# Kernel tuning notes

Measured on AMD Instinct MI355X. Metric: run time of the kernel, lower is better.

Reference implementation:

```python
import jax, jax.numpy as jnp
import numpy as np
from math import sqrt

N_PATCHES = 128
ATTENTION_WINDOW = 10
NEG_FILL = -10000.0


def _mask(L):
    # pid[i] = patch index of position i; channels = L // n_patches
    channels = L // N_PATCHES
    pid = jnp.repeat(jnp.arange(N_PATCHES), channels)
    diff = pid[None, :] - pid[:, None]  # diff[i, j] = pid[j] - pid[i]
    return (diff <= 0) | (diff >= ATTENTION_WINDOW)  # True = masked


def setup_inputs() -> dict:
    key = jax.random.key(0)
    k1, k2, k3 = jax.random.split(key, 3)
    B, H, L, D = 4, 8, 2048, 64
    return {
        "queries": jax.random.normal(k1, (B, H, L, D), dtype=jnp.float32),
        "keys": jax.random.normal(k2, (B, H, L, D), dtype=jnp.float32),
        "values": jax.random.normal(k3, (B, H, L, D), dtype=jnp.float32),
        "log_scale": jnp.asarray(np.log(2.0), dtype=jnp.float32),
    }


def reference(queries, keys, values, log_scale):
    B, H, L, D = queries.shape
    scores = jnp.einsum("bhqd,bhkd->bhqk", queries, keys)
    scale = jnp.clip(jnp.exp(log_scale), 1.0, 30.0) / sqrt(D)
    cmask = _mask(L)[None, None]  # [1,1,L,L]
    pos = jnp.where(cmask, NEG_FILL, scores)
    neg = jnp.where(cmask, NEG_FILL, -scores)
    A = jax.nn.softmax(scale * pos, axis=-1) - jax.nn.softmax(scale * neg, axis=-1)
    return jnp.einsum("bhqk,bhkd->bhqd", A, values)
```

## Files before the change

kernel.cpp:

```cpp
#include <hip/hip_runtime.h>
#include <hip/hip_bf16.h>


#define LSEQ   2048
#define DIM    64
#define CH     16
#define WIN    9
#define GRP    8
#define VCOLS  272

#define SK 72
#define SV 280
#define SA 168
#define UNELEMS 21504

typedef __attribute__((ext_vector_type(8))) short bf16x8;
typedef __attribute__((ext_vector_type(4))) float f32x4;

__device__ __forceinline__ unsigned short f2bf1(float a) {
  unsigned int u = __float_as_uint(a);
  u = (u + 0x7fffu + ((u >> 16) & 1u)) >> 16;
  return (unsigned short)u;
}

__device__ __forceinline__ unsigned int pack2bf(float a, float b) {
  unsigned int ua = __float_as_uint(a);
  unsigned int ub = __float_as_uint(b);
  ua = (ua + 0x7fffu + ((ua >> 16) & 1u)) >> 16;
  ub = (ub + 0x7fffu + ((ub >> 16) & 1u)) & 0xffff0000u;
  return ua | ub;
}

__device__ __forceinline__ bf16x8 pack8(float4 a, float4 b) {
  bf16x8 r;
  r[0] = (short)f2bf1(a.x); r[1] = (short)f2bf1(a.y);
  r[2] = (short)f2bf1(a.z); r[3] = (short)f2bf1(a.w);
  r[4] = (short)f2bf1(b.x); r[5] = (short)f2bf1(b.y);
  r[6] = (short)f2bf1(b.z); r[7] = (short)f2bf1(b.w);
  return r;
}

__global__ __launch_bounds__(512, 4)
void signed_attn_kernel(const float* __restrict__ Q,
                        const float* __restrict__ K,
                        const float* __restrict__ V,
                        const float* __restrict__ LS,
                        float* __restrict__ O) {
  __shared__ __align__(16) unsigned short Vt[DIM * SV];
  __shared__ __align__(16) unsigned short Un[UNELEMS];

  const int g  = blockIdx.x & 15;
  const int bh = blockIdx.x >> 4;
  const int t  = threadIdx.x;
  const int p0 = g * GRP;

  const int kbp = (127 - p0) < 16 ? (127 - p0) : 16;
  const int kb  = kbp * CH;

  const float4* Kg = (const float4*)(K + ((size_t)bh * LSEQ + (size_t)(p0 + 1) * CH) * DIM);
  const float4* Vg = (const float4*)(V + ((size_t)bh * LSEQ + (size_t)(p0 + 1) * CH) * DIM);

  for (int e = t; e < kb * 16; e += 512) {
    int row = e >> 4, d4 = e & 15;
    float4 v = Kg[e];
    *(uint2*)&Un[row * SK + d4 * 4] =
        make_uint2(pack2bf(v.x, v.y), pack2bf(v.z, v.w));
  }
  {
    const int nq = kb >> 2;
    for (int e = t; e < nq * 16; e += 512) {
      int cq = e >> 4, d4 = e & 15;
      int c = cq << 2;
      float4 v0 = Vg[(c + 0) * 16 + d4];
      float4 v1 = Vg[(c + 1) * 16 + d4];
      float4 v2 = Vg[(c + 2) * 16 + d4];
      float4 v3 = Vg[(c + 3) * 16 + d4];
      int db = d4 << 2;
      *(uint2*)&Vt[(db + 0) * SV + c] = make_uint2(pack2bf(v0.x, v1.x), pack2bf(v2.x, v3.x));
      *(uint2*)&Vt[(db + 1) * SV + c] = make_uint2(pack2bf(v0.y, v1.y), pack2bf(v2.y, v3.y));
      *(uint2*)&Vt[(db + 2) * SV + c] = make_uint2(pack2bf(v0.z, v1.z), pack2bf(v2.z, v3.z));
      *(uint2*)&Vt[(db + 3) * SV + c] = make_uint2(pack2bf(v0.w, v1.w), pack2bf(v2.w, v3.w));
    }
  }
  for (int c = kb + (t >> 6); c < VCOLS; c += 8) Vt[(t & 63) * SV + c] = 0;

  const int w  = t >> 6;
  const int l  = t & 63;
  const int lr = l & 15;
  const int q4 = l >> 4;

  const int p   = p0 + w;
  const int npk = (127 - p) < WIN ? (127 - p) : WIN;

  const float* Qg = Q + ((size_t)bh * LSEQ + (size_t)p * CH) * DIM;
  bf16x8 qa[2];
#pragma unroll
  for (int s = 0; s < 2; s++) {
    const float* qp = Qg + lr * DIM + q4 * 8 + 32 * s;
    qa[s] = pack8(*(const float4*)qp, *(const float4*)(qp + 4));
  }

  const float scale = fminf(30.f, fmaxf(1.f, __expf(LS[0]))) * 0.125f;
  const int koff = w * CH;

  __syncthreads();

  f32x4 sacc[WIN];
#pragma unroll
  for (int tl = 0; tl < WIN; tl++) {
    f32x4 acc = {0.f, 0.f, 0.f, 0.f};
#pragma unroll
    for (int s = 0; s < 2; s++) {
      bf16x8 b = *(const bf16x8*)&Un[(koff + tl * 16 + lr) * SK + q4 * 8 + 32 * s];
      acc = __builtin_amdgcn_mfma_f32_16x16x32_bf16(qa[s], b, acc, 0, 0, 0);
    }
    sacc[tl] = acc;
  }

  __syncthreads();

  float sp[4] = {0.f, 0.f, 0.f, 0.f}, sn[4] = {0.f, 0.f, 0.f, 0.f};
#pragma unroll
  for (int tl = 0; tl < WIN; tl++) {
    bool val = tl < npk;
#pragma unroll
    for (int r = 0; r < 4; r++) {
      float x  = scale * sacc[tl][r];
      float e1 = __expf(x);
      float e2 = __builtin_amdgcn_rcpf(e1);
      sacc[tl][r] = e1;
      sp[r] += val ? e1 : 0.f;
      sn[r] += val ? e2 : 0.f;
    }
  }
#pragma unroll
  for (int off = 1; off < 16; off <<= 1)
#pragma unroll
    for (int r = 0; r < 4; r++) {
      sp[r] += __shfl_xor(sp[r], off);
      sn[r] += __shfl_xor(sn[r], off);
    }
  float rp[4], rn[4];
#pragma unroll
  for (int r = 0; r < 4; r++) {
    rp[r] = __builtin_amdgcn_rcpf(sp[r]);
    rn[r] = __builtin_amdgcn_rcpf(sn[r]);
  }

  unsigned short* Aw = Un + w * 16 * SA;
#pragma unroll
  for (int tl = 0; tl < WIN; tl++) {
    bool val = tl < npk;
#pragma unroll
    for (int r = 0; r < 4; r++) {
      float e1 = sacc[tl][r];
      float a  = val ? (e1 * rp[r] - __builtin_amdgcn_rcpf(e1) * rn[r]) : 0.f;
      Aw[(q4 * 4 + r) * SA + tl * 16 + lr] = f2bf1(a);
    }
  }
#pragma unroll
  for (int r = 0; r < 4; r++)
    Aw[(q4 * 4 + r) * SA + 144 + lr] = 0;

  f32x4 oacc[4] = {{0,0,0,0},{0,0,0,0},{0,0,0,0},{0,0,0,0}};
#pragma unroll
  for (int s = 0; s < 5; s++) {
    bf16x8 a = *(const bf16x8*)&Aw[lr * SA + s * 32 + q4 * 8];
#pragma unroll
    for (int n = 0; n < 4; n++) {
      bf16x8 b = *(const bf16x8*)&Vt[(n * 16 + lr) * SV + koff + s * 32 + q4 * 8];
      oacc[n] = __builtin_amdgcn_mfma_f32_16x16x32_bf16(a, b, oacc[n], 0, 0, 0);
    }
  }

  float* Og = O + ((size_t)bh * LSEQ + (size_t)p * CH) * DIM;
  const bool live = (npk > 0);
#pragma unroll
  for (int n = 0; n < 4; n++)
#pragma unroll
    for (int r = 0; r < 4; r++)
      Og[(q4 * 4 + r) * DIM + n * 16 + lr] = live ? oacc[n][r] : 0.f;
}

extern "C" void kernel_launch(void* const* d_in, const int* in_sizes, int n_in,
                              void* d_out, int out_size, void* d_ws, size_t ws_size,
                              hipStream_t stream) {
  const float* Q  = (const float*)d_in[0];
  const float* K  = (const float*)d_in[1];
  const float* V  = (const float*)d_in[2];
  const float* LS = (const float*)d_in[3];
  float* O = (float*)d_out;
  signed_attn_kernel<<<dim3(512), dim3(512), 0, stream>>>(Q, K, V, LS, O);
}
```

Baseline: 101.2 us.

## Defer softmax normalization to after PV matmul and compute row sums via MFMA

Stores unnormalized bf16 exp(x) in shared memory and rebuilds the negative branch by taking reciprocals of those bf16 values. Row sums come from MFMA against a ones vector. Two separate PV accumulations are normalized in the epilogue. This removes the cross-lane shuffle reduction and the per-element normalization before the matmul, at the cost of doubling the PV MFMAs and reducing accuracy because reciprocals are taken of rounded values. Float-to-bf16 rounding is also simplified from round-to-nearest-even to round-half-up.

```diff
diff --git a/kernel.cpp b/kernel.cpp
--- a/kernel.cpp
+++ b/kernel.cpp
@@ -17,27 +17,21 @@
 typedef __attribute__((ext_vector_type(8))) short bf16x8;
 typedef __attribute__((ext_vector_type(4))) float f32x4;
 
-__device__ __forceinline__ unsigned short f2bf1(float a) {
-  unsigned int u = __float_as_uint(a);
-  u = (u + 0x7fffu + ((u >> 16) & 1u)) >> 16;
-  return (unsigned short)u;
-}
+union BF8 { bf16x8 v; unsigned int u[4]; };
 
-__device__ __forceinline__ unsigned int pack2bf(float a, float b) {
-  unsigned int ua = __float_as_uint(a);
-  unsigned int ub = __float_as_uint(b);
-  ua = (ua + 0x7fffu + ((ua >> 16) & 1u)) >> 16;
-  ub = (ub + 0x7fffu + ((ub >> 16) & 1u)) & 0xffff0000u;
+__device__ __forceinline__ unsigned int bfpack(float a, float b) {
+  unsigned int ua = (__float_as_uint(a) + 0x8000u) >> 16;
+  unsigned int ub = (__float_as_uint(b) + 0x8000u) & 0xFFFF0000u;
   return ua | ub;
 }
 
 __device__ __forceinline__ bf16x8 pack8(float4 a, float4 b) {
-  bf16x8 r;
-  r[0] = (short)f2bf1(a.x); r[1] = (short)f2bf1(a.y);
-  r[2] = (short)f2bf1(a.z); r[3] = (short)f2bf1(a.w);
-  r[4] = (short)f2bf1(b.x); r[5] = (short)f2bf1(b.y);
-  r[6] = (short)f2bf1(b.z); r[7] = (short)f2bf1(b.w);
-  return r;
+  BF8 r;
+  r.u[0] = bfpack(a.x, a.y);
+  r.u[1] = bfpack(a.z, a.w);
+  r.u[2] = bfpack(b.x, b.y);
+  r.u[3] = bfpack(b.z, b.w);
+  return r.v;
 }
 
 __global__ __launch_bounds__(512, 4)
@@ -63,8 +57,7 @@
   for (int e = t; e < kb * 16; e += 512) {
     int row = e >> 4, d4 = e & 15;
     float4 v = Kg[e];
-    *(uint2*)&Un[row * SK + d4 * 4] =
-        make_uint2(pack2bf(v.x, v.y), pack2bf(v.z, v.w));
+    *(uint2*)&Un[row * SK + d4 * 4] = make_uint2(bfpack(v.x, v.y), bfpack(v.z, v.w));
   }
   {
     const int nq = kb >> 2;
@@ -76,10 +69,10 @@
       float4 v2 = Vg[(c + 2) * 16 + d4];
       float4 v3 = Vg[(c + 3) * 16 + d4];
       int db = d4 << 2;
-      *(uint2*)&Vt[(db + 0) * SV + c] = make_uint2(pack2bf(v0.x, v1.x), pack2bf(v2.x, v3.x));
-      *(uint2*)&Vt[(db + 1) * SV + c] = make_uint2(pack2bf(v0.y, v1.y), pack2bf(v2.y, v3.y));
-      *(uint2*)&Vt[(db + 2) * SV + c] = make_uint2(pack2bf(v0.z, v1.z), pack2bf(v2.z, v3.z));
-      *(uint2*)&Vt[(db + 3) * SV + c] = make_uint2(pack2bf(v0.w, v1.w), pack2bf(v2.w, v3.w));
+      *(uint2*)&Vt[(db + 0) * SV + c] = make_uint2(bfpack(v0.x, v1.x), bfpack(v2.x, v3.x));
+      *(uint2*)&Vt[(db + 1) * SV + c] = make_uint2(bfpack(v0.y, v1.y), bfpack(v2.y, v3.y));
+      *(uint2*)&Vt[(db + 2) * SV + c] = make_uint2(bfpack(v0.z, v1.z), bfpack(v2.z, v3.z));
+      *(uint2*)&Vt[(db + 3) * SV + c] = make_uint2(bfpack(v0.w, v1.w), bfpack(v2.w, v3.w));
     }
   }
   for (int c = kb + (t >> 6); c < VCOLS; c += 8) Vt[(t & 63) * SV + c] = 0;
@@ -119,67 +112,66 @@
 
   __syncthreads();
 
-  float sp[4] = {0.f, 0.f, 0.f, 0.f}, sn[4] = {0.f, 0.f, 0.f, 0.f};
-#pragma unroll
-  for (int tl = 0; tl < WIN; tl++) {
-    bool val = tl < npk;
-#pragma unroll
-    for (int r = 0; r < 4; r++) {
-      float x  = scale * sacc[tl][r];
-      float e1 = __expf(x);
-      float e2 = __builtin_amdgcn_rcpf(e1);
-      sacc[tl][r] = e1;
-      sp[r] += val ? e1 : 0.f;
-      sn[r] += val ? e2 : 0.f;
-    }
-  }
-#pragma unroll
-  for (int off = 1; off < 16; off <<= 1)
-#pragma unroll
-    for (int r = 0; r < 4; r++) {
-      sp[r] += __shfl_xor(sp[r], off);
-      sn[r] += __shfl_xor(sn[r], off);
-    }
-  float rp[4], rn[4];
-#pragma unroll
-  for (int r = 0; r < 4; r++) {
-    rp[r] = __builtin_amdgcn_rcpf(sp[r]);
-    rn[r] = __builtin_amdgcn_rcpf(sn[r]);
-  }
-
   unsigned short* Aw = Un + w * 16 * SA;
 #pragma unroll
   for (int tl = 0; tl < WIN; tl++) {
-    bool val = tl < npk;
+    const bool val = tl < npk;
 #pragma unroll
     for (int r = 0; r < 4; r++) {
-      float e1 = sacc[tl][r];
-      float a  = val ? (e1 * rp[r] - __builtin_amdgcn_rcpf(e1) * rn[r]) : 0.f;
-      Aw[(q4 * 4 + r) * SA + tl * 16 + lr] = f2bf1(a);
+      float e1 = __expf(scale * sacc[tl][r]);
+      unsigned int u = (__float_as_uint(e1) + 0x8000u) >> 16;
+      Aw[(q4 * 4 + r) * SA + tl * 16 + lr] = (unsigned short)(val ? u : 0u);
     }
   }
 #pragma unroll
   for (int r = 0; r < 4; r++)
     Aw[(q4 * 4 + r) * SA + 144 + lr] = 0;
 
-  f32x4 oacc[4] = {{0,0,0,0},{0,0,0,0},{0,0,0,0},{0,0,0,0}};
+  BF8 bones;
+#pragma unroll
+  for (int j = 0; j < 4; j++) bones.u[j] = 0x3F803F80u;
+
+  f32x4 o1[4] = {{0,0,0,0},{0,0,0,0},{0,0,0,0},{0,0,0,0}};
+  f32x4 o2[4] = {{0,0,0,0},{0,0,0,0},{0,0,0,0},{0,0,0,0}};
+  f32x4 s1 = {0,0,0,0}, s2 = {0,0,0,0};
+
 #pragma unroll
   for (int s = 0; s < 5; s++) {
-    bf16x8 a = *(const bf16x8*)&Aw[lr * SA + s * 32 + q4 * 8];
+    BF8 a1, a2;
+    a1.v = *(const bf16x8*)&Aw[lr * SA + s * 32 + q4 * 8];
+#pragma unroll
+    for (int j = 0; j < 4; j++) {
+      unsigned int d    = a1.u[j];
+      unsigned int lo16 = d << 16;
+      unsigned int hi16 = d & 0xFFFF0000u;
+      float lo = __uint_as_float(lo16);
+      float hi = __uint_as_float(hi16);
+      float rl = (lo16 == 0u) ? 0.f : __builtin_amdgcn_rcpf(lo);
+      float rh = (hi16 == 0u) ? 0.f : __builtin_amdgcn_rcpf(hi);
+      a2.u[j] = bfpack(rl, rh);
+    }
+    s1 = __builtin_amdgcn_mfma_f32_16x16x32_bf16(a1.v, bones.v, s1, 0, 0, 0);
+    s2 = __builtin_amdgcn_mfma_f32_16x16x32_bf16(a2.v, bones.v, s2, 0, 0, 0);
 #pragma unroll
     for (int n = 0; n < 4; n++) {
       bf16x8 b = *(const bf16x8*)&Vt[(n * 16 + lr) * SV + koff + s * 32 + q4 * 8];
-      oacc[n] = __builtin_amdgcn_mfma_f32_16x16x32_bf16(a, b, oacc[n], 0, 0, 0);
+      o1[n] = __builtin_amdgcn_mfma_f32_16x16x32_bf16(a1.v, b, o1[n], 0, 0, 0);
+      o2[n] = __builtin_amdgcn_mfma_f32_16x16x32_bf16(a2.v, b, o2[n], 0, 0, 0);
     }
   }
 
   float* Og = O + ((size_t)bh * LSEQ + (size_t)p * CH) * DIM;
   const bool live = (npk > 0);
 #pragma unroll
-  for (int n = 0; n < 4; n++)
+  for (int r = 0; r < 4; r++) {
+    float rp = __builtin_amdgcn_rcpf(s1[r]);
+    float rn = __builtin_amdgcn_rcpf(s2[r]);
 #pragma unroll
-    for (int r = 0; r < 4; r++)
-      Og[(q4 * 4 + r) * DIM + n * 16 + lr] = live ? oacc[n][r] : 0.f;
+    for (int n = 0; n < 4; n++) {
+      float o = o1[n][r] * rp - o2[n][r] * rn;
+      Og[(q4 * 4 + r) * DIM + n * 16 + lr] = live ? o : 0.f;
+    }
+  }
 }
 
 extern "C" void kernel_launch(void* const* d_in, const int* in_sizes, int n_in,
```

Measured after the change: 102.0 us. No clear change (+0.8%).
